# Kernel optimization log

Hardware: AMD Instinct MI355X
Metric: run time of the kernel (lower is better)

The kernel has to match this reference:

```python
import jax, jax.numpy as jnp
import numpy as np

KH, KW = 2, 2  # kernel_shape: stride-2 zero-insertion unpool

def setup_inputs() -> dict:
    key = jax.random.key(0)
    x = jax.random.normal(key, (32, 112, 112, 64), dtype=jnp.float32)
    return {"x": x}

def reference(x) -> jnp.ndarray:
    # Equivalent to conv2d_transpose with identity-in-top-left kernel and
    # stride (KH, KW): each input element goes to the top-left of a KHxKW
    # zero block. Output shape: [B, H*KH, W*KW, C].
    b, h, w, c = x.shape
    out = jnp.zeros((b, h * KH, w * KW, c), dtype=x.dtype)
    out = out.at[:, ::KH, ::KW, :].set(x)
    return out
```

## Files before the change

### kernel.cpp

```cpp
#include <hip/hip_runtime.h>

typedef float f4 __attribute__((ext_vector_type(4)));

__global__ __launch_bounds__(256) void unpool_scatter_deep(
    const f4* __restrict__ x, f4* __restrict__ out) {
    const int tid = threadIdx.x;

#pragma unroll 4
    for (int r = blockIdx.x; r < 3584; r += 896) {
        const f4* __restrict__ xrow = x + (size_t)r * 1792;
        f4* __restrict__ orow = out + (size_t)(2 * r) * 3584;

#pragma unroll
        for (int k = 0; k < 7; ++k) {
            const int j = k * 256 + tid;
            const f4 v = xrow[j];
            const int o = ((j & ~15) << 1) | (j & 15);
            orow[o] = v;
        }
    }
}

extern "C" void kernel_launch(void* const* d_in, const int* in_sizes, int n_in,
                              void* d_out, int out_size, void* d_ws, size_t ws_size,
                              hipStream_t stream) {
    hipMemsetAsync(d_out, 0, (size_t)out_size, stream);

    dim3 grid(896);
    dim3 block(256);
    unpool_scatter_deep<<<grid, block, 0, stream>>>((const f4*)d_in[0], (f4*)d_out);
}
```

Before: 431.6 us.

## Replace full memset plus scatter with odd-row zeroing and dense even-row expansion

Drops the memset over the whole output and instead zeroes only the odd output rows in one kernel. A second kernel writes each even row densely, interleaving input values with zeros, so every output byte is written exactly once. Loads and stores are marked nontemporal to avoid cache pollution. This removes the redundant write traffic on even rows, at the cost of two launches and a more intricate per-thread index mapping.

```diff
diff --git a/kernel.cpp b/kernel.cpp
--- a/kernel.cpp
+++ b/kernel.cpp
@@ -2,31 +2,46 @@
 
 typedef float f4 __attribute__((ext_vector_type(4)));
 
-__global__ __launch_bounds__(256) void unpool_scatter_deep(
+__global__ __launch_bounds__(256) void zero_odd_rows(f4* __restrict__ out) {
+    f4* __restrict__ row = out + (size_t)(2 * blockIdx.x + 1) * 3584;
+    const f4 z = (f4){0.f, 0.f, 0.f, 0.f};
+#pragma unroll
+    for (int k = 0; k < 14; ++k) {
+        __builtin_nontemporal_store(z, &row[k * 256 + threadIdx.x]);
+    }
+}
+
+__global__ __launch_bounds__(256) void expand_even_rows(
     const f4* __restrict__ x, f4* __restrict__ out) {
     const int tid = threadIdx.x;
+    const int r   = blockIdx.x;
 
-#pragma unroll 4
-    for (int r = blockIdx.x; r < 3584; r += 896) {
-        const f4* __restrict__ xrow = x + (size_t)r * 1792;
-        f4* __restrict__ orow = out + (size_t)(2 * r) * 3584;
+    const f4* __restrict__ xrow = x + (size_t)r * 1792;
+    f4* __restrict__ orow = out + (size_t)(2 * r) * 3584;
 
+    const int low  = ((tid >> 5) << 4) | (tid & 15);
+    const int half = (tid & 16) << 3;
+    const bool hi  = (tid & 16) != 0;
+
+    f4 v[7];
 #pragma unroll
-        for (int k = 0; k < 7; ++k) {
-            const int j = k * 256 + tid;
-            const f4 v = xrow[j];
-            const int o = ((j & ~15) << 1) | (j & 15);
-            orow[o] = v;
-        }
+    for (int m = 0; m < 7; ++m) {
+        v[m] = __builtin_nontemporal_load(&xrow[m * 256 + half + low]);
+    }
+
+    const f4 z = (f4){0.f, 0.f, 0.f, 0.f};
+#pragma unroll
+    for (int m = 0; m < 7; ++m) {
+        __builtin_nontemporal_store(hi ? z : v[m], &orow[512 * m + tid]);
+        __builtin_nontemporal_store(hi ? v[m] : z,
+                                    &orow[512 * m + 256 + (tid ^ 16)]);
     }
 }
 
 extern "C" void kernel_launch(void* const* d_in, const int* in_sizes, int n_in,
                               void* d_out, int out_size, void* d_ws, size_t ws_size,
                               hipStream_t stream) {
-    hipMemsetAsync(d_out, 0, (size_t)out_size, stream);
-
-    dim3 grid(896);
-    dim3 block(256);
-    unpool_scatter_deep<<<grid, block, 0, stream>>>((const f4*)d_in[0], (f4*)d_out);
+    f4* out = (f4*)d_out;
+    zero_odd_rows<<<dim3(3584), dim3(256), 0, stream>>>(out);
+    expand_even_rows<<<dim3(3584), dim3(256), 0, stream>>>((const f4*)d_in[0], out);
 }
```

After: 462.2 us. 7.1% more time.
